# Optimization experiments

Measured on AMD Instinct MI355X. Metric: run time of the kernel, lower is better.

The kernel has to match this reference:

```python
import jax, jax.numpy as jnp
import numpy as np

HORIZON = 1024
N_EMBD = 256
N_LAYER = 4
ACTION_DIM = 10
DIM = 64
ACT_NUM = 10
N_POS = 4 * (1 + HORIZON)
FEAT = 3 + DIM * ACT_NUM + ACTION_DIM  # 653
EPS = 1e-5
BATCH = 8


def _layernorm(x, g, b):
    m = jnp.mean(x, axis=-1, keepdims=True)
    v = jnp.mean((x - m) ** 2, axis=-1, keepdims=True)
    return (x - m) * jax.lax.rsqrt(v + EPS) * g + b


def setup_inputs() -> dict:
    key = jax.random.key(0)
    ks = jax.random.split(key, 16)
    f = jnp.float32
    L, E = N_LAYER, N_EMBD
    return {
        'query_states': jax.random.normal(ks[0], (BATCH, 64), f),
        'action_set': jax.random.normal(ks[1], (BATCH, ACT_NUM, DIM), f),
        'context_actions': jax.random.normal(ks[2], (BATCH, HORIZON, ACTION_DIM), f),
        'context_rewards': jax.random.normal(ks[3], (BATCH, HORIZON, 1), f),
        'W_embed': jax.random.normal(ks[4], (FEAT, E), f) * 0.02,
        'b_embed': jnp.zeros((E,), f),
        'wpe': jax.random.normal(ks[5], (N_POS, E), f) * 0.02,
        'Wq': jax.random.normal(ks[6], (L, E, E), f) * 0.02,
        'Wk': jax.random.normal(ks[7], (L, E, E), f) * 0.02,
        'Wv': jax.random.normal(ks[8], (L, E, E), f) * 0.02,
        'ln1_g': jnp.ones((L, E), f),
        'ln1_b': jnp.zeros((L, E), f),
        'W1': jax.random.normal(ks[9], (L, E, E), f) * 0.02,
        'b1': jnp.zeros((L, E), f),
        'W2': jax.random.normal(ks[10], (L, E, E), f) * 0.02,
        'b2': jnp.zeros((L, E), f),
        'ln2_g': jnp.ones((L, E), f),
        'ln2_b': jnp.zeros((L, E), f),
        'W_pred': jax.random.normal(ks[11], (E, ACTION_DIM), f) * 0.02,
        'b_pred': jnp.zeros((ACTION_DIM,), f),
    }


def reference(query_states, action_set, context_actions, context_rewards,
              W_embed, b_embed, wpe, Wq, Wk, Wv,
              ln1_g, ln1_b, W1, b1, W2, b2, ln2_g, ln2_b,
              W_pred, b_pred):
    B = action_set.shape[0]
    T = context_actions.shape[1]
    A = context_actions.shape[2]
    N = 2 * T
    # --- build the interleaved sequence (test=False path) ---
    aset0 = action_set.reshape(B, 1, -1)                         # [B,1,dim*act_num]
    aset = jnp.concatenate([aset0, jnp.zeros_like(aset0)], axis=1)  # [B,2,F0]
    aset = jnp.tile(aset, (1, T, 1))                              # [B,2T,F0]
    action_seq = jnp.zeros((B, N, A + 1), dtype=context_actions.dtype)
    action_seq = action_seq.at[:, 1::2, :].set(
        jnp.concatenate([context_actions, context_rewards], axis=2))
    one_seq = jnp.ones((B, N, 1), dtype=context_actions.dtype)
    pos_seq = jnp.broadcast_to(
        jnp.arange(1, N + 1, dtype=context_actions.dtype).reshape(1, N, 1), (B, N, 1))
    seq = jnp.concatenate([aset, action_seq, one_seq, pos_seq], axis=2)  # [B,N,FEAT]
    # --- embed + positional embedding ---
    H = seq @ W_embed + b_embed          # [B,N,E]
    H = H + wpe[:N]                       # position_ids = arange(N)
    # --- causal mask with per-row 1/(i+1) normalization ---
    i = jnp.arange(N)[:, None]
    j = jnp.arange(N)[None, :]
    mask = jnp.where(j <= i, 1.0 / (i + 1).astype(H.dtype), 0.0)  # [N,N]
    # --- decoder layers: relu(QK^T)*mask attention + MLP, layernorms ---
    for l in range(N_LAYER):
        q = H @ Wq[l]
        k = H @ Wk[l]
        v = H @ Wv[l]
        attn = jax.nn.relu(jnp.einsum('bid,bjd->bij', q, k)) * mask  # [B,N,N]
        H = H + jnp.einsum('bij,bjd->bid', attn, v)
        H = _layernorm(H, ln1_g[l], ln1_b[l])
        H = H + jax.nn.relu(H @ W1[l] + b1[l]) @ W2[l] + b2[l]
        H = _layernorm(H, ln2_g[l], ln2_b[l])
    preds = H @ W_pred + b_pred           # [B,N,action_dim]
    return preds[:, 0::2, :]              # [B,T,action_dim]
```

## Files before the change

kernel.cpp:

```cpp
#include <hip/hip_runtime.h>


#define BB 8
#define TT 1024
#define NN 2048
#define EE 256
#define LL 4

typedef __attribute__((ext_vector_type(8))) short short8;
typedef __attribute__((ext_vector_type(4))) float f32x4;

__device__ inline ushort f2b(float f) {
    union { float f; unsigned u; } x; x.f = f;
    unsigned u = x.u;
    return (ushort)((u + 0x7fffu + ((u >> 16) & 1u)) >> 16);
}
__device__ inline unsigned cvtpk(float lo, float hi) {
    unsigned r;
    asm volatile("v_cvt_pk_bf16_f32 %0, %1, %2" : "=v"(r) : "v"(lo), "v"(hi));
    return r;
}
__device__ inline size_t pk256(int row, int k) {
    return ((size_t)((row >> 4) * 8 + (k >> 5))) * 512
         + (size_t)((((k >> 3) & 3) * 16 + (row & 15)) * 8 + (k & 7));
}
__device__ inline size_t vpk_idx(int bb, int nn, int e) {
    return ((size_t)(bb*64 + (nn >> 5)) * 16 + (e >> 4)) * 512
         + (size_t)((((nn >> 3) & 3) * 16 + (e & 15)) * 8 + (nn & 7));
}

__global__ __launch_bounds__(256) void wprep_k(
    const float* __restrict__ Wq, const float* __restrict__ Wk,
    const float* __restrict__ Wv, const float* __restrict__ W1,
    const float* __restrict__ W2,
    ushort* __restrict__ WQKt, ushort* __restrict__ WVt,
    ushort* __restrict__ W1t, ushort* __restrict__ W2t)
{
    int id = blockIdx.x;
    int m = id >> 4, t = id & 15;
    int l = m / 5, which = m % 5;
    const float* src; ushort* dst;
    size_t o = (size_t)l * 65536;
    switch (which) {
        case 0: src = Wq + o; dst = WQKt + (size_t)l*131072;          break;
        case 1: src = Wk + o; dst = WQKt + (size_t)l*131072 + 65536;  break;
        case 2: src = Wv + o; dst = WVt + o; break;
        case 3: src = W1 + o; dst = W1t + o; break;
        default: src = W2 + o; dst = W2t + o; break;
    }
    int tk = (t >> 2) * 64;
    int tn = (t & 3) * 64;
    __shared__ ushort T[64][68];
    int tid = threadIdx.x;
    int r = tid >> 4, c4 = (tid & 15) * 4;
    #pragma unroll
    for (int it = 0; it < 4; ++it) {
        int k = r + it*16;
        float4 v = *(const float4*)&src[(size_t)(tk + k)*256 + tn + c4];
        T[k][c4+0] = f2b(v.x); T[k][c4+1] = f2b(v.y);
        T[k][c4+2] = f2b(v.z); T[k][c4+3] = f2b(v.w);
    }
    __syncthreads();
    #pragma unroll
    for (int it = 0; it < 4; ++it) {
        int n = tn + r + it*16;
        int k0 = tk + c4;
        ushort4 ov;
        ov.x = T[c4+0][n-tn]; ov.y = T[c4+1][n-tn];
        ov.z = T[c4+2][n-tn]; ov.w = T[c4+3][n-tn];
        *(ushort4*)&dst[pk256(n, k0)] = ov;
    }
}

__global__ __launch_bounds__(256) void base_even_k(
    const float* __restrict__ aset, const float* __restrict__ We,
    const float* __restrict__ be, float* __restrict__ BE)
{
    int b = blockIdx.x; int e = threadIdx.x;
    __shared__ float as[640];
    for (int i = e; i < 640; i += 256) as[i] = aset[b*640 + i];
    __syncthreads();
    float s = We[651*EE + e] + be[e];
    for (int f = 0; f < 640; ++f) s = fmaf(as[f], We[f*EE + e], s);
    BE[b*EE + e] = s;
}

__global__ __launch_bounds__(256) void embed_k(
    const float* __restrict__ BE, const float* __restrict__ ca,
    const float* __restrict__ cr, const float* __restrict__ We,
    const float* __restrict__ be, const float* __restrict__ wpe,
    float* __restrict__ H, ushort* __restrict__ Hbf)
{
    int e = threadIdx.x;
    #pragma unroll
    for (int k = 0; k < 8; ++k) {
        int rb = blockIdx.x * 8 + k;
        int b = rb >> 11, n = rb & (NN-1);
        float h;
        if ((n & 1) == 0) {
            h = BE[b*EE + e];
        } else {
            int t = n >> 1;
            h = We[651*EE + e] + be[e];
            const float* cap = ca + (size_t)(b*TT + t)*10;
            #pragma unroll
            for (int i = 0; i < 10; ++i) h = fmaf(cap[i], We[(640+i)*EE + e], h);
            h = fmaf(cr[b*TT + t], We[650*EE + e], h);
        }
        h = fmaf((float)(n + 1), We[652*EE + e], h);
        h += wpe[(size_t)n*EE + e];
        H[(size_t)rb*EE + e] = h;
        Hbf[pk256(rb, e)] = f2b(h);
    }
}

__global__ __launch_bounds__(256, 2) void qkv_k(
    const ushort* __restrict__ A, const ushort* __restrict__ WQK,
    const ushort* __restrict__ WV,
    ushort* __restrict__ Qo, ushort* __restrict__ Ko, ushort* __restrict__ Vo)
{
    int tid = threadIdx.x;
    int w = tid >> 6, l = tid & 63;
    int lr = l & 15, lg = l >> 4;
    int wr = w >> 1, wc = w & 1;
    int rt0 = blockIdx.x * 8 + wr*4;
    int ct0 = blockIdx.y * 8 + wc*4;
    const ushort* Ap = A + (size_t)rt0*4096 + l*8;
    const ushort* Bp = (blockIdx.y < 4 ? WQK + (size_t)ct0*4096
                                       : WV + (size_t)(ct0-32)*4096) + l*8;
    f32x4 acc[4][4];
    #pragma unroll
    for (int i = 0; i < 4; ++i)
        #pragma unroll
        for (int j = 0; j < 4; ++j) acc[i][j] = (f32x4){0.f,0.f,0.f,0.f};
    #pragma unroll
    for (int kc = 0; kc < 8; ++kc) {
        short8 af[4], bf[4];
        #pragma unroll
        for (int rg = 0; rg < 4; ++rg) af[rg] = *(const short8*)(Ap + (size_t)rg*4096 + kc*512);
        #pragma unroll
        for (int cg = 0; cg < 4; ++cg) bf[cg] = *(const short8*)(Bp + (size_t)cg*4096 + kc*512);
        #pragma unroll
        for (int rg = 0; rg < 4; ++rg)
            #pragma unroll
            for (int cg = 0; cg < 4; ++cg)
                acc[rg][cg] = __builtin_amdgcn_mfma_f32_16x16x32_bf16(af[rg], bf[cg], acc[rg][cg], 0,0,0);
    }
    #pragma unroll
    for (int rg = 0; rg < 4; ++rg)
        #pragma unroll
        for (int cg = 0; cg < 4; ++cg)
            #pragma unroll
            for (int r = 0; r < 4; ++r) {
                int row = rt0*16 + rg*16 + lg*4 + r;
                int col = ct0*16 + cg*16 + lr;
                ushort xv = f2b(acc[rg][cg][r]);
                if (col < 256)      Qo[pk256(row, col)] = xv;
                else if (col < 512) Ko[pk256(row, col - 256)] = xv;
                else {
                    int e = col - 512, bb = row >> 11, nn = row & (NN-1);
                    Vo[vpk_idx(bb, nn, e)] = xv;
                }
            }
}

__global__ __launch_bounds__(256, 2) void mlp1_k(
    const ushort* __restrict__ A, const ushort* __restrict__ Bw,
    const float* __restrict__ bias, ushort* __restrict__ Cv)
{
    int tid = threadIdx.x;
    int w = tid >> 6, l = tid & 63;
    int lr = l & 15, lg = l >> 4;
    int wr = w >> 1, wc = w & 1;
    int rt0 = blockIdx.x * 8 + wr*4;
    int ct0 = blockIdx.y * 8 + wc*4;
    const ushort* Ap = A  + (size_t)rt0*4096 + l*8;
    const ushort* Bp = Bw + (size_t)ct0*4096 + l*8;
    f32x4 acc[4][4];
    #pragma unroll
    for (int i = 0; i < 4; ++i)
        #pragma unroll
        for (int j = 0; j < 4; ++j) acc[i][j] = (f32x4){0.f,0.f,0.f,0.f};
    #pragma unroll
    for (int kc = 0; kc < 8; ++kc) {
        short8 af[4], bf[4];
        #pragma unroll
        for (int rg = 0; rg < 4; ++rg) af[rg] = *(const short8*)(Ap + (size_t)rg*4096 + kc*512);
        #pragma unroll
        for (int cg = 0; cg < 4; ++cg) bf[cg] = *(const short8*)(Bp + (size_t)cg*4096 + kc*512);
        #pragma unroll
        for (int rg = 0; rg < 4; ++rg)
            #pragma unroll
            for (int cg = 0; cg < 4; ++cg)
                acc[rg][cg] = __builtin_amdgcn_mfma_f32_16x16x32_bf16(af[rg], bf[cg], acc[rg][cg], 0,0,0);
    }
    #pragma unroll
    for (int rg = 0; rg < 4; ++rg)
        #pragma unroll
        for (int cg = 0; cg < 4; ++cg)
            #pragma unroll
            for (int r = 0; r < 4; ++r) {
                int row = rt0*16 + rg*16 + lg*4 + r;
                int col = ct0*16 + cg*16 + lr;
                float x = fmaxf(acc[rg][cg][r] + bias[col], 0.f);
                Cv[pk256(row, col)] = f2b(x);
            }
}

__global__ __launch_bounds__(256, 2) void mlp2ln_k(
    const ushort* __restrict__ A, const ushort* __restrict__ Bw,
    const float* __restrict__ bias, const float* __restrict__ Res,
    const float* __restrict__ g, const float* __restrict__ bt,
    float* __restrict__ Hout, ushort* __restrict__ Hpk)
{
    int tid = threadIdx.x;
    int w = tid >> 6, l = tid & 63;
    int lr = l & 15, lg = l >> 4;
    int rt0 = blockIdx.x * 2;
    int ct0 = w * 4;
    const ushort* Ap = A  + (size_t)rt0*4096 + l*8;
    const ushort* Bp = Bw + (size_t)ct0*4096 + l*8;
    f32x4 acc[2][4];
    #pragma unroll
    for (int i = 0; i < 2; ++i)
        #pragma unroll
        for (int j = 0; j < 4; ++j) acc[i][j] = (f32x4){0.f,0.f,0.f,0.f};
    #pragma unroll
    for (int kc = 0; kc < 8; ++kc) {
        short8 a0 = *(const short8*)(Ap + kc*512);
        short8 a1 = *(const short8*)(Ap + 4096 + kc*512);
        short8 bf[4];
        #pragma unroll
        for (int cg = 0; cg < 4; ++cg) bf[cg] = *(const short8*)(Bp + (size_t)cg*4096 + kc*512);
        #pragma unroll
        for (int cg = 0; cg < 4; ++cg) {
            acc[0][cg] = __builtin_amdgcn_mfma_f32_16x16x32_bf16(a0, bf[cg], acc[0][cg], 0,0,0);
            acc[1][cg] = __builtin_amdgcn_mfma_f32_16x16x32_bf16(a1, bf[cg], acc[1][cg], 0,0,0);
        }
    }
    __shared__ float red[32][4][2];
    float sm[2][4] = {}, sq[2][4] = {};
    #pragma unroll
    for (int rg = 0; rg < 2; ++rg)
        #pragma unroll
        for (int cg = 0; cg < 4; ++cg)
            #pragma unroll
            for (int r = 0; r < 4; ++r) {
                int grow = blockIdx.x*32 + rg*16 + lg*4 + r;
                int col = w*64 + cg*16 + lr;
                float v = acc[rg][cg][r] + bias[col] + Res[(size_t)grow*EE + col];
                acc[rg][cg][r] = v;
                sm[rg][r] += v; sq[rg][r] += v*v;
            }
    #pragma unroll
    for (int off = 1; off < 16; off <<= 1)
        #pragma unroll
        for (int rg = 0; rg < 2; ++rg)
            #pragma unroll
            for (int r = 0; r < 4; ++r) {
                sm[rg][r] += __shfl_xor(sm[rg][r], off);
                sq[rg][r] += __shfl_xor(sq[rg][r], off);
            }
    if (lr == 0) {
        #pragma unroll
        for (int rg = 0; rg < 2; ++rg)
            #pragma unroll
            for (int r = 0; r < 4; ++r) {
                int rl = rg*16 + lg*4 + r;
                red[rl][w][0] = sm[rg][r];
                red[rl][w][1] = sq[rg][r];
            }
    }
    __syncthreads();
    #pragma unroll
    for (int rg = 0; rg < 2; ++rg)
        #pragma unroll
        for (int r = 0; r < 4; ++r) {
            int rl = rg*16 + lg*4 + r;
            float S  = red[rl][0][0] + red[rl][1][0] + red[rl][2][0] + red[rl][3][0];
            float S2 = red[rl][0][1] + red[rl][1][1] + red[rl][2][1] + red[rl][3][1];
            float mean = S * (1.0f/256.0f);
            float var  = S2 * (1.0f/256.0f) - mean*mean;
            float inv  = 1.0f / sqrtf(var + 1e-5f);
            int grow = blockIdx.x*32 + rl;
            #pragma unroll
            for (int cg = 0; cg < 4; ++cg) {
                int col = w*64 + cg*16 + lr;
                float y = (acc[rg][cg][r] - mean) * inv * g[col] + bt[col];
                Hout[(size_t)grow*EE + col] = y;
                Hpk[pk256(grow, col)] = f2b(y);
            }
        }
}

__global__ __launch_bounds__(512, 2) void attn_k(
    const ushort* __restrict__ Qp, const ushort* __restrict__ Kp,
    const ushort* __restrict__ Vp, const float* __restrict__ H,
    const float* __restrict__ g, const float* __restrict__ bt,
    float* __restrict__ Xout, ushort* __restrict__ Lpk)
{
    int blk = blockIdx.x;
    int pk = blk >> 3, b = blk & 7;
    int tid = threadIdx.x;
    int w = tid >> 6, l = tid & 63;
    int lr = l & 15, lg = l >> 4;
    int sel  = (w & 1) ^ ((w >> 2) & 1);
    int part = w >> 1;
    int s  = sel ? (127 - pk) : pk;
    int i0 = s * 16;
    int NT = (s >> 1) + 1;
    int j0 = (part * NT) >> 2;
    int j1 = ((part + 1) * NT) >> 2;

    __shared__ float comb[2][5440];

    const ushort* Qt    = Qp + (size_t)(b*128 + s) * 4096 + l*8;
    const ushort* Kbase = Kp + (size_t)(b*128) * 4096 + l*8;
    const ushort* Vbase = Vp + (size_t)(b*64) * 16 * 512 + l*8;

    short8 qb[8];
    #pragma unroll
    for (int kc = 0; kc < 8; ++kc) qb[kc] = *(const short8*)(Qt + kc*512);

    f32x4 oacc[16];
    #pragma unroll
    for (int et = 0; et < 16; ++et) oacc[et] = (f32x4){0.f,0.f,0.f,0.f};

    int ig = i0 + lr;
    for (int jt = j0; jt < j1; ++jt) {
        const ushort* Kt = Kbase + (size_t)(jt*2) * 4096;
        short8 ka0[8], ka1[8];
        #pragma unroll
        for (int kc = 0; kc < 8; ++kc) {
            ka0[kc] = *(const short8*)(Kt + kc*512);
            ka1[kc] = *(const short8*)(Kt + 4096 + kc*512);
        }
        const ushort* Vt = Vbase + (size_t)(jt*16) * 512;
        short8 vf[16];
        #pragma unroll
        for (int et = 0; et < 16; ++et)
            vf[et] = *(const short8*)(Vt + et*512);
        f32x4 c0a = {0.f,0.f,0.f,0.f}, c0b = {0.f,0.f,0.f,0.f};
        f32x4 c1a = {0.f,0.f,0.f,0.f}, c1b = {0.f,0.f,0.f,0.f};
        #pragma unroll
        for (int kc = 0; kc < 8; kc += 2) {
            c0a = __builtin_amdgcn_mfma_f32_16x16x32_bf16(ka0[kc],   qb[kc],   c0a, 0,0,0);
            c0b = __builtin_amdgcn_mfma_f32_16x16x32_bf16(ka0[kc+1], qb[kc+1], c0b, 0,0,0);
            c1a = __builtin_amdgcn_mfma_f32_16x16x32_bf16(ka1[kc],   qb[kc],   c1a, 0,0,0);
            c1b = __builtin_amdgcn_mfma_f32_16x16x32_bf16(ka1[kc+1], qb[kc+1], c1b, 0,0,0);
        }
        f32x4 c0 = c0a + c0b, c1 = c1a + c1b;
        #pragma unroll
        for (int r = 0; r < 4; ++r) {
            int jg = jt*32 + lg*4 + r;
            c0[r] = (jg <= ig) ? fmaxf(c0[r], 0.f) : 0.f;
            c1[r] = (jg + 16 <= ig) ? fmaxf(c1[r], 0.f) : 0.f;
        }
        unsigned u0 = cvtpk(c0[0], c0[1]), u1 = cvtpk(c0[2], c0[3]);
        unsigned u2 = cvtpk(c1[0], c1[1]), u3 = cvtpk(c1[2], c1[3]);
        int srcA = 32*(lg & 1) + lr;
        int srcB = srcA + 16;
        unsigned a0A = __shfl((int)u0, srcA), a1A = __shfl((int)u1, srcA);
        unsigned a0B = __shfl((int)u0, srcB), a1B = __shfl((int)u1, srcB);
        unsigned b0A = __shfl((int)u2, srcA), b1A = __shfl((int)u3, srcA);
        unsigned b0B = __shfl((int)u2, srcB), b1B = __shfl((int)u3, srcB);
        bool lo = (lg < 2);
        union { unsigned u[4]; short8 v; } sv;
        sv.u[0] = lo ? a0A : b0A;
        sv.u[1] = lo ? a1A : b1A;
        sv.u[2] = lo ? a0B : b0B;
        sv.u[3] = lo ? a1B : b1B;
        short8 sa = sv.v;
        __builtin_amdgcn_s_setprio(1);
        #pragma unroll
        for (int et = 0; et < 16; ++et)
            oacc[et] = __builtin_amdgcn_mfma_f32_16x16x32_bf16(sa, vf[et], oacc[et], 0,0,0);
        __builtin_amdgcn_s_setprio(0);
    }

    float* cb = &comb[sel][0];
    #pragma unroll
    for (int rnd = 1; rnd <= 3; ++rnd) {
        if (part == rnd) {
            #pragma unroll
            for (int et = 0; et < 16; ++et)
                #pragma unroll
                for (int r = 0; r < 4; ++r) {
                    int idx = et*340 + l*5 + r;
                    float v = oacc[et][r];
                    if (rnd == 1) cb[idx] = v; else cb[idx] += v;
                }
        }
        __syncthreads();
    }
    if (part == 0) {
        float sm[4] = {0.f,0.f,0.f,0.f}, sq[4] = {0.f,0.f,0.f,0.f};
        #pragma unroll
        for (int et = 0; et < 16; ++et)
            #pragma unroll
            for (int r = 0; r < 4; ++r) {
                int irow = i0 + lg*4 + r;
                size_t base = ((size_t)(b*NN + irow))*EE + et*16 + lr;
                float x = H[base] + (oacc[et][r] + cb[et*340 + l*5 + r])
                                    * (1.0f / (float)(irow + 1));
                oacc[et][r] = x;
                sm[r] += x; sq[r] += x*x;
            }
        #pragma unroll
        for (int off = 1; off < 16; off <<= 1)
            #pragma unroll
            for (int r = 0; r < 4; ++r) {
                sm[r] += __shfl_xor(sm[r], off);
                sq[r] += __shfl_xor(sq[r], off);
            }
        float mean[4], inv[4];
        #pragma unroll
        for (int r = 0; r < 4; ++r) {
            mean[r] = sm[r] * (1.0f/256.0f);
            float var = sq[r] * (1.0f/256.0f) - mean[r]*mean[r];
            inv[r] = 1.0f / sqrtf(var + 1e-5f);
        }
        #pragma unroll
        for (int et = 0; et < 16; ++et) {
            int col = et*16 + lr;
            float gv = g[col], bv = bt[col];
            #pragma unroll
            for (int r = 0; r < 4; ++r) {
                int irow = i0 + lg*4 + r;
                size_t base = ((size_t)(b*NN + irow))*EE + col;
                float y = (oacc[et][r] - mean[r]) * inv[r] * gv + bv;
                Xout[base] = y;
                Lpk[pk256(b*NN + irow, col)] = f2b(y);
            }
        }
    }
}

__global__ __launch_bounds__(256) void pred_k(
    const float* __restrict__ H, const float* __restrict__ Wp,
    const float* __restrict__ bp, float* __restrict__ out)
{
    int bt = blockIdx.x;
    int b = bt >> 10, t = bt & 1023;
    size_t row = (size_t)b*NN + 2*t;
    __shared__ float hs[256];
    __shared__ float pr[16][16];
    int tid = threadIdx.x;
    hs[tid] = H[row*EE + tid];
    __syncthreads();
    int c = tid & 15, seg = tid >> 4;
    float p = 0.f;
    if (c < 10) {
        #pragma unroll
        for (int e2 = 0; e2 < 16; ++e2)
            p = fmaf(hs[seg*16 + e2], Wp[(seg*16 + e2)*10 + c], p);
    }
    pr[seg][c] = p;
    __syncthreads();
    if (tid < 10) {
        float sacc = bp[tid];
        #pragma unroll
        for (int k2 = 0; k2 < 16; ++k2) sacc += pr[k2][tid];
        out[(size_t)bt*10 + tid] = sacc;
    }
}

extern "C" void kernel_launch(void* const* d_in, const int* in_sizes, int n_in,
                              void* d_out, int out_size, void* d_ws, size_t ws_size,
                              hipStream_t stream)
{
    const float* action_set = (const float*)d_in[1];
    const float* ctx_act    = (const float*)d_in[2];
    const float* ctx_rew    = (const float*)d_in[3];
    const float* W_embed    = (const float*)d_in[4];
    const float* b_embed    = (const float*)d_in[5];
    const float* wpe        = (const float*)d_in[6];
    const float* Wq         = (const float*)d_in[7];
    const float* Wk         = (const float*)d_in[8];
    const float* Wv         = (const float*)d_in[9];
    const float* ln1g       = (const float*)d_in[10];
    const float* ln1b       = (const float*)d_in[11];
    const float* W1         = (const float*)d_in[12];
    const float* b1         = (const float*)d_in[13];
    const float* W2         = (const float*)d_in[14];
    const float* b2         = (const float*)d_in[15];
    const float* ln2g       = (const float*)d_in[16];
    const float* ln2b       = (const float*)d_in[17];
    const float* Wp         = (const float*)d_in[18];
    const float* bp         = (const float*)d_in[19];
    float* out = (float*)d_out;

    float* ws = (float*)d_ws;
    const size_t SZ = (size_t)BB*NN*EE;
    size_t o = 0;
    float*  Hb   = ws;               o += SZ;
    float*  Xb   = ws + o;           o += SZ;
    ushort* Hbf  = (ushort*)(ws+o);  o += SZ/2;
    ushort* Qp   = (ushort*)(ws+o);  o += SZ/2;
    ushort* Kpk  = (ushort*)(ws+o);  o += SZ/2;
    ushort* Vpk  = (ushort*)(ws+o);  o += SZ/2;
    ushort* WQKt = (ushort*)(ws+o);  o += 262144;
    ushort* WVt  = (ushort*)(ws+o);  o += 131072;
    ushort* W1t  = (ushort*)(ws+o);  o += 131072;
    ushort* W2t  = (ushort*)(ws+o);  o += 131072;
    float*  BE   = ws + o;

    wprep_k<<<320, 256, 0, stream>>>(Wq, Wk, Wv, W1, W2, WQKt, WVt, W1t, W2t);
    base_even_k<<<BB, 256, 0, stream>>>(action_set, W_embed, b_embed, BE);
    embed_k<<<BB*NN/8, 256, 0, stream>>>(BE, ctx_act, ctx_rew, W_embed, b_embed, wpe, Hb, Hbf);

    for (int l = 0; l < LL; ++l) {
        qkv_k<<<dim3(128, 6), 256, 0, stream>>>(
            Hbf, WQKt + (size_t)l*131072, WVt + (size_t)l*65536, Qp, Kpk, Vpk);
        attn_k<<<512, 512, 0, stream>>>(
            Qp, Kpk, Vpk, Hb, ln1g + l*EE, ln1b + l*EE, Xb, Hbf);
        mlp1_k<<<dim3(128, 2), 256, 0, stream>>>(
            Hbf, W1t + (size_t)l*65536, b1 + l*EE, Qp);
        mlp2ln_k<<<512, 256, 0, stream>>>(
            Qp, W2t + (size_t)l*65536, b2 + l*EE, Xb,
            ln2g + l*EE, ln2b + l*EE, Hb, Hbf);
    }
    pred_k<<<BB*TT, 256, 0, stream>>>(Hb, Wp, bp, out);
}
```

Before: 446.3 us.

## Split causal attention into two halves and move residual+LayerNorm into separate kernel

The attention kernel changes from 512-thread blocks with four waves splitting the key range and combining through shared memory to 256-thread blocks. Each block now covers a 64-row query group, and its key range is cut into two halves written to two fp32 partial buffers. A new comb_ln1_k kernel adds the partials, applies the 1/(i+1) scale and residual, and does LayerNorm with vectorized loads. This removes the in-block shared-memory reduction and its barriers and rebalances work across blocks. In exchange it adds an extra kernel launch per layer and two full fp32 activation round trips through global memory, and puts a __syncthreads inside the key loop.

```diff
diff --git a/kernel.cpp b/kernel.cpp
--- a/kernel.cpp
+++ b/kernel.cpp
@@ -293,30 +293,27 @@
         }
 }
 
-__global__ __launch_bounds__(512, 2) void attn_k(
+__global__ __launch_bounds__(256, 2) void attn_k(
     const ushort* __restrict__ Qp, const ushort* __restrict__ Kp,
-    const ushort* __restrict__ Vp, const float* __restrict__ H,
-    const float* __restrict__ g, const float* __restrict__ bt,
-    float* __restrict__ Xout, ushort* __restrict__ Lpk)
-{
-    int blk = blockIdx.x;
-    int pk = blk >> 3, b = blk & 7;
+    const ushort* __restrict__ Vp, float* __restrict__ Oa,
+    float* __restrict__ Ob)
+{
+    int bi = blockIdx.x;
+    int h = bi >> 8;
+    int j = bi & 255;
+    int b = j >> 5;
+    int p = h ? (31 - (j & 31)) : (j & 31);
     int tid = threadIdx.x;
     int w = tid >> 6, l = tid & 63;
     int lr = l & 15, lg = l >> 4;
-    int sel  = (w & 1) ^ ((w >> 2) & 1);
-    int part = w >> 1;
-    int s  = sel ? (127 - pk) : pk;
-    int i0 = s * 16;
-    int NT = (s >> 1) + 1;
-    int j0 = (part * NT) >> 2;
-    int j1 = ((part + 1) * NT) >> 2;
-
-    __shared__ float comb[2][5440];
-
-    const ushort* Qt    = Qp + (size_t)(b*128 + s) * 4096 + l*8;
-    const ushort* Kbase = Kp + (size_t)(b*128) * 4096 + l*8;
-    const ushort* Vbase = Vp + (size_t)(b*64) * 16 * 512 + l*8;
+    int i0 = p*64 + w*16;
+    int j0 = h ? (p + 1) : 0;
+    int j1 = h ? (2*p + 2) : (p + 1);
+    float* Op = h ? Ob : Oa;
+
+    const ushort* Qt    = Qp + (size_t)(b*128 + p*4 + w)*4096 + l*8;
+    const ushort* Kbase = Kp + (size_t)(b*128)*4096 + l*8;
+    const ushort* Vbase = Vp + (size_t)(b*64)*16*512 + l*8;
 
     short8 qb[8];
     #pragma unroll
@@ -376,64 +373,53 @@
         for (int et = 0; et < 16; ++et)
             oacc[et] = __builtin_amdgcn_mfma_f32_16x16x32_bf16(sa, vf[et], oacc[et], 0,0,0);
         __builtin_amdgcn_s_setprio(0);
-    }
-
-    float* cb = &comb[sel][0];
-    #pragma unroll
-    for (int rnd = 1; rnd <= 3; ++rnd) {
-        if (part == rnd) {
-            #pragma unroll
-            for (int et = 0; et < 16; ++et)
-                #pragma unroll
-                for (int r = 0; r < 4; ++r) {
-                    int idx = et*340 + l*5 + r;
-                    float v = oacc[et][r];
-                    if (rnd == 1) cb[idx] = v; else cb[idx] += v;
-                }
-        }
         __syncthreads();
     }
-    if (part == 0) {
-        float sm[4] = {0.f,0.f,0.f,0.f}, sq[4] = {0.f,0.f,0.f,0.f};
-        #pragma unroll
-        for (int et = 0; et < 16; ++et)
-            #pragma unroll
-            for (int r = 0; r < 4; ++r) {
-                int irow = i0 + lg*4 + r;
-                size_t base = ((size_t)(b*NN + irow))*EE + et*16 + lr;
-                float x = H[base] + (oacc[et][r] + cb[et*340 + l*5 + r])
-                                    * (1.0f / (float)(irow + 1));
-                oacc[et][r] = x;
-                sm[r] += x; sq[r] += x*x;
-            }
-        #pragma unroll
-        for (int off = 1; off < 16; off <<= 1)
-            #pragma unroll
-            for (int r = 0; r < 4; ++r) {
-                sm[r] += __shfl_xor(sm[r], off);
-                sq[r] += __shfl_xor(sq[r], off);
-            }
-        float mean[4], inv[4];
+    #pragma unroll
+    for (int et = 0; et < 16; ++et)
         #pragma unroll
         for (int r = 0; r < 4; ++r) {
-            mean[r] = sm[r] * (1.0f/256.0f);
-            float var = sq[r] * (1.0f/256.0f) - mean[r]*mean[r];
-            inv[r] = 1.0f / sqrtf(var + 1e-5f);
-        }
-        #pragma unroll
-        for (int et = 0; et < 16; ++et) {
-            int col = et*16 + lr;
-            float gv = g[col], bv = bt[col];
-            #pragma unroll
-            for (int r = 0; r < 4; ++r) {
-                int irow = i0 + lg*4 + r;
-                size_t base = ((size_t)(b*NN + irow))*EE + col;
-                float y = (oacc[et][r] - mean[r]) * inv[r] * gv + bv;
-                Xout[base] = y;
-                Lpk[pk256(b*NN + irow, col)] = f2b(y);
-            }
-        }
-    }
+            int irow = i0 + lg*4 + r;
+            Op[((size_t)(b*NN + irow))*EE + et*16 + lr] = oacc[et][r];
+        }
+}
+
+__global__ __launch_bounds__(256) void comb_ln1_k(
+    const float* Oa, const float* __restrict__ Ob,
+    const float* __restrict__ H, const float* __restrict__ g,
+    const float* __restrict__ bt, float* Xout, ushort* __restrict__ Lpk)
+{
+    int w = threadIdx.x >> 6, l = threadIdx.x & 63;
+    size_t row = (size_t)blockIdx.x*4 + w;
+    float sc = 1.0f / (float)((row & (NN-1)) + 1);
+    float4 oa = *(const float4*)&Oa[row*EE + l*4];
+    float4 ob = *(const float4*)&Ob[row*EE + l*4];
+    float4 hh = *(const float4*)&H[row*EE + l*4];
+    float4 x;
+    x.x = hh.x + (oa.x + ob.x)*sc;
+    x.y = hh.y + (oa.y + ob.y)*sc;
+    x.z = hh.z + (oa.z + ob.z)*sc;
+    x.w = hh.w + (oa.w + ob.w)*sc;
+    float s  = x.x + x.y + x.z + x.w;
+    float s2 = x.x*x.x + x.y*x.y + x.z*x.z + x.w*x.w;
+    #pragma unroll
+    for (int off = 1; off < 64; off <<= 1) {
+        s  += __shfl_xor(s,  off);
+        s2 += __shfl_xor(s2, off);
+    }
+    float mean = s * (1.0f/256.0f);
+    float var  = s2 * (1.0f/256.0f) - mean*mean;
+    float inv  = 1.0f / sqrtf(var + 1e-5f);
+    float4 gv = *(const float4*)&g[l*4];
+    float4 bv = *(const float4*)&bt[l*4];
+    float4 y;
+    y.x = (x.x - mean)*inv*gv.x + bv.x;
+    y.y = (x.y - mean)*inv*gv.y + bv.y;
+    y.z = (x.z - mean)*inv*gv.z + bv.z;
+    y.w = (x.w - mean)*inv*gv.w + bv.w;
+    *(float4*)&Xout[row*EE + l*4] = y;
+    ushort4 yb; yb.x = f2b(y.x); yb.y = f2b(y.y); yb.z = f2b(y.z); yb.w = f2b(y.w);
+    *(ushort4*)&Lpk[pk256((int)row, l*4)] = yb;
 }
 
 __global__ __launch_bounds__(256) void pred_k(
@@ -495,6 +481,7 @@
     size_t o = 0;
     float*  Hb   = ws;               o += SZ;
     float*  Xb   = ws + o;           o += SZ;
+    float*  Obuf = ws + o;           o += SZ;
     ushort* Hbf  = (ushort*)(ws+o);  o += SZ/2;
     ushort* Qp   = (ushort*)(ws+o);  o += SZ/2;
     ushort* Kpk  = (ushort*)(ws+o);  o += SZ/2;
@@ -512,8 +499,9 @@
     for (int l = 0; l < LL; ++l) {
         qkv_k<<<dim3(128, 6), 256, 0, stream>>>(
             Hbf, WQKt + (size_t)l*131072, WVt + (size_t)l*65536, Qp, Kpk, Vpk);
-        attn_k<<<512, 512, 0, stream>>>(
-            Qp, Kpk, Vpk, Hb, ln1g + l*EE, ln1b + l*EE, Xb, Hbf);
+        attn_k<<<512, 256, 0, stream>>>(Qp, Kpk, Vpk, Xb, Obuf);
+        comb_ln1_k<<<BB*NN/4, 256, 0, stream>>>(
+            Xb, Obuf, Hb, ln1g + l*EE, ln1b + l*EE, Xb, Hbf);
         mlp1_k<<<dim3(128, 2), 256, 0, stream>>>(
             Hbf, W1t + (size_t)l*65536, b1 + l*EE, Qp);
         mlp2ln_k<<<512, 256, 0, stream>>>(
```

Measured after the change: 490.6 us. 1.1x slower.

## Restructure attention so four row-waves share key/value tiles in lockstep

Applied to the files above, without the earlier changes.

The attention kernel now gives each block 64 consecutive query rows: four waves of 16 rows, with two halves splitting the causal key range. Previously each block paired a short and a long 16-row strip across four key-range partitions. A barrier inside the key loop keeps the four waves on the same K/V tile, so loads can be reused through cache, and the cross-partition reduction becomes a single LDS exchange. The grid is halved, launch bounds allow one block per CU, and the old short/long pairing is gone, so per-block work now grows with row position and the load may be unbalanced.

```diff
diff --git a/kernel.cpp b/kernel.cpp
--- a/kernel.cpp
+++ b/kernel.cpp
@@ -293,30 +293,26 @@
         }
 }
 
-__global__ __launch_bounds__(512, 2) void attn_k(
+__global__ __launch_bounds__(512, 1) void attn_k(
     const ushort* __restrict__ Qp, const ushort* __restrict__ Kp,
     const ushort* __restrict__ Vp, const float* __restrict__ H,
     const float* __restrict__ g, const float* __restrict__ bt,
     float* __restrict__ Xout, ushort* __restrict__ Lpk)
 {
     int blk = blockIdx.x;
-    int pk = blk >> 3, b = blk & 7;
+    int p = blk >> 3, b = blk & 7;
     int tid = threadIdx.x;
     int w = tid >> 6, l = tid & 63;
     int lr = l & 15, lg = l >> 4;
-    int sel  = (w & 1) ^ ((w >> 2) & 1);
-    int part = w >> 1;
-    int s  = sel ? (127 - pk) : pk;
-    int i0 = s * 16;
-    int NT = (s >> 1) + 1;
-    int j0 = (part * NT) >> 2;
-    int j1 = ((part + 1) * NT) >> 2;
-
-    __shared__ float comb[2][5440];
-
-    const ushort* Qt    = Qp + (size_t)(b*128 + s) * 4096 + l*8;
-    const ushort* Kbase = Kp + (size_t)(b*128) * 4096 + l*8;
-    const ushort* Vbase = Vp + (size_t)(b*64) * 16 * 512 + l*8;
+    int h = w >> 2, w4 = w & 3;
+    int i0 = p*64 + w4*16;
+    int jbase = h * (p + 1);
+
+    __shared__ float comb[4][16][256];
+
+    const ushort* Qt    = Qp + (size_t)(b*128 + p*4 + w4)*4096 + l*8;
+    const ushort* Kbase = Kp + (size_t)(b*128)*4096 + l*8;
+    const ushort* Vbase = Vp + (size_t)(b*64)*16*512 + l*8;
 
     short8 qb[8];
     #pragma unroll
@@ -327,15 +323,16 @@
     for (int et = 0; et < 16; ++et) oacc[et] = (f32x4){0.f,0.f,0.f,0.f};
 
     int ig = i0 + lr;
-    for (int jt = j0; jt < j1; ++jt) {
-        const ushort* Kt = Kbase + (size_t)(jt*2) * 4096;
+    for (int jt = 0; jt <= p; ++jt) {
+        int jte = jbase + jt;
+        const ushort* Kt = Kbase + (size_t)(jte*2) * 4096;
         short8 ka0[8], ka1[8];
         #pragma unroll
         for (int kc = 0; kc < 8; ++kc) {
             ka0[kc] = *(const short8*)(Kt + kc*512);
             ka1[kc] = *(const short8*)(Kt + 4096 + kc*512);
         }
-        const ushort* Vt = Vbase + (size_t)(jt*16) * 512;
+        const ushort* Vt = Vbase + (size_t)(jte*16) * 512;
         short8 vf[16];
         #pragma unroll
         for (int et = 0; et < 16; ++et)
@@ -352,7 +349,7 @@
         f32x4 c0 = c0a + c0b, c1 = c1a + c1b;
         #pragma unroll
         for (int r = 0; r < 4; ++r) {
-            int jg = jt*32 + lg*4 + r;
+            int jg = jte*32 + lg*4 + r;
             c0[r] = (jg <= ig) ? fmaxf(c0[r], 0.f) : 0.f;
             c1[r] = (jg + 16 <= ig) ? fmaxf(c1[r], 0.f) : 0.f;
         }
@@ -376,24 +373,18 @@
         for (int et = 0; et < 16; ++et)
             oacc[et] = __builtin_amdgcn_mfma_f32_16x16x32_bf16(sa, vf[et], oacc[et], 0,0,0);
         __builtin_amdgcn_s_setprio(0);
-    }
-
-    float* cb = &comb[sel][0];
-    #pragma unroll
-    for (int rnd = 1; rnd <= 3; ++rnd) {
-        if (part == rnd) {
-            #pragma unroll
-            for (int et = 0; et < 16; ++et)
-                #pragma unroll
-                for (int r = 0; r < 4; ++r) {
-                    int idx = et*340 + l*5 + r;
-                    float v = oacc[et][r];
-                    if (rnd == 1) cb[idx] = v; else cb[idx] += v;
-                }
-        }
         __syncthreads();
     }
-    if (part == 0) {
+
+    if (h == 1) {
+        #pragma unroll
+        for (int et = 0; et < 16; ++et)
+            #pragma unroll
+            for (int r = 0; r < 4; ++r)
+                comb[w4][lg*4 + r][et*16 + lr] = oacc[et][r];
+    }
+    __syncthreads();
+    if (h == 0) {
         float sm[4] = {0.f,0.f,0.f,0.f}, sq[4] = {0.f,0.f,0.f,0.f};
         #pragma unroll
         for (int et = 0; et < 16; ++et)
@@ -401,8 +392,8 @@
             for (int r = 0; r < 4; ++r) {
                 int irow = i0 + lg*4 + r;
                 size_t base = ((size_t)(b*NN + irow))*EE + et*16 + lr;
-                float x = H[base] + (oacc[et][r] + cb[et*340 + l*5 + r])
-                                    * (1.0f / (float)(irow + 1));
+                float o = oacc[et][r] + comb[w4][lg*4 + r][et*16 + lr];
+                float x = H[base] + o * (1.0f / (float)(irow + 1));
                 oacc[et][r] = x;
                 sm[r] += x; sq[r] += x*x;
             }
@@ -512,7 +503,7 @@
     for (int l = 0; l < LL; ++l) {
         qkv_k<<<dim3(128, 6), 256, 0, stream>>>(
             Hbf, WQKt + (size_t)l*131072, WVt + (size_t)l*65536, Qp, Kpk, Vpk);
-        attn_k<<<512, 512, 0, stream>>>(
+        attn_k<<<256, 512, 0, stream>>>(
             Qp, Kpk, Vpk, Hb, ln1g + l*EE, ln1b + l*EE, Xb, Hbf);
         mlp1_k<<<dim3(128, 2), 256, 0, stream>>>(
             Hbf, W1t + (size_t)l*65536, b1 + l*EE, Qp);
```

Measured after the change: 546.9 us. +22.6%, slower.

## Process 32 query rows per wave in attention to reuse K/V fragments

Applied to the files above, without the earlier changes.

The attention kernel now gives each wave two 16-row query tiles (32 rows) instead of one, so every K and V fragment loaded from global memory feeds twice as many MFMAs. The grid is halved to 256 blocks, and the shared-memory combine buffer is resized and re-laid-out row-major for 32 rows. K and V are now loaded inside the MFMA loops rather than preloaded into registers. The intent is to halve K/V traffic per unit of work, at the cost of twice the accumulator registers (possible spills or lower occupancy), fewer blocks for the GPU's CUs, and less latency hiding.

```diff
diff --git a/kernel.cpp b/kernel.cpp
--- a/kernel.cpp
+++ b/kernel.cpp
@@ -306,75 +306,90 @@
     int lr = l & 15, lg = l >> 4;
     int sel  = (w & 1) ^ ((w >> 2) & 1);
     int part = w >> 1;
-    int s  = sel ? (127 - pk) : pk;
-    int i0 = s * 16;
-    int NT = (s >> 1) + 1;
+    int z  = sel ? (63 - pk) : pk;
+    int i0 = z * 32;
+    int NT = z + 1;
     int j0 = (part * NT) >> 2;
     int j1 = ((part + 1) * NT) >> 2;
 
-    __shared__ float comb[2][5440];
-
-    const ushort* Qt    = Qp + (size_t)(b*128 + s) * 4096 + l*8;
+    __shared__ float comb[2][32 * 260];
+
+    const ushort* Qt    = Qp + (size_t)(b*128 + z*2) * 4096 + l*8;
     const ushort* Kbase = Kp + (size_t)(b*128) * 4096 + l*8;
     const ushort* Vbase = Vp + (size_t)(b*64) * 16 * 512 + l*8;
 
-    short8 qb[8];
-    #pragma unroll
-    for (int kc = 0; kc < 8; ++kc) qb[kc] = *(const short8*)(Qt + kc*512);
-
-    f32x4 oacc[16];
-    #pragma unroll
-    for (int et = 0; et < 16; ++et) oacc[et] = (f32x4){0.f,0.f,0.f,0.f};
-
-    int ig = i0 + lr;
+    short8 qa[8], qb[8];
+    #pragma unroll
+    for (int kc = 0; kc < 8; ++kc) {
+        qa[kc] = *(const short8*)(Qt + kc*512);
+        qb[kc] = *(const short8*)(Qt + 4096 + kc*512);
+    }
+
+    f32x4 oa[16], ob[16];
+    #pragma unroll
+    for (int et = 0; et < 16; ++et) {
+        oa[et] = (f32x4){0.f,0.f,0.f,0.f};
+        ob[et] = (f32x4){0.f,0.f,0.f,0.f};
+    }
+
+    int ig0 = i0 + lr;
+    int ig1 = i0 + 16 + lr;
     for (int jt = j0; jt < j1; ++jt) {
         const ushort* Kt = Kbase + (size_t)(jt*2) * 4096;
-        short8 ka0[8], ka1[8];
+        const ushort* Vt = Vbase + (size_t)(jt*16) * 512;
+        f32x4 c0 = {0.f,0.f,0.f,0.f}, c1 = {0.f,0.f,0.f,0.f};
+        f32x4 d0 = {0.f,0.f,0.f,0.f}, d1 = {0.f,0.f,0.f,0.f};
         #pragma unroll
         for (int kc = 0; kc < 8; ++kc) {
-            ka0[kc] = *(const short8*)(Kt + kc*512);
-            ka1[kc] = *(const short8*)(Kt + 4096 + kc*512);
-        }
-        const ushort* Vt = Vbase + (size_t)(jt*16) * 512;
-        short8 vf[16];
-        #pragma unroll
-        for (int et = 0; et < 16; ++et)
-            vf[et] = *(const short8*)(Vt + et*512);
-        f32x4 c0a = {0.f,0.f,0.f,0.f}, c0b = {0.f,0.f,0.f,0.f};
-        f32x4 c1a = {0.f,0.f,0.f,0.f}, c1b = {0.f,0.f,0.f,0.f};
-        #pragma unroll
-        for (int kc = 0; kc < 8; kc += 2) {
-            c0a = __builtin_amdgcn_mfma_f32_16x16x32_bf16(ka0[kc],   qb[kc],   c0a, 0,0,0);
-            c0b = __builtin_amdgcn_mfma_f32_16x16x32_bf16(ka0[kc+1], qb[kc+1], c0b, 0,0,0);
-            c1a = __builtin_amdgcn_mfma_f32_16x16x32_bf16(ka1[kc],   qb[kc],   c1a, 0,0,0);
-            c1b = __builtin_amdgcn_mfma_f32_16x16x32_bf16(ka1[kc+1], qb[kc+1], c1b, 0,0,0);
-        }
-        f32x4 c0 = c0a + c0b, c1 = c1a + c1b;
+            short8 k0 = *(const short8*)(Kt + kc*512);
+            short8 k1 = *(const short8*)(Kt + 4096 + kc*512);
+            c0 = __builtin_amdgcn_mfma_f32_16x16x32_bf16(k0, qa[kc], c0, 0,0,0);
+            c1 = __builtin_amdgcn_mfma_f32_16x16x32_bf16(k1, qa[kc], c1, 0,0,0);
+            d0 = __builtin_amdgcn_mfma_f32_16x16x32_bf16(k0, qb[kc], d0, 0,0,0);
+            d1 = __builtin_amdgcn_mfma_f32_16x16x32_bf16(k1, qb[kc], d1, 0,0,0);
+        }
         #pragma unroll
         for (int r = 0; r < 4; ++r) {
             int jg = jt*32 + lg*4 + r;
-            c0[r] = (jg <= ig) ? fmaxf(c0[r], 0.f) : 0.f;
-            c1[r] = (jg + 16 <= ig) ? fmaxf(c1[r], 0.f) : 0.f;
-        }
+            c0[r] = (jg <= ig0)      ? fmaxf(c0[r], 0.f) : 0.f;
+            c1[r] = (jg + 16 <= ig0) ? fmaxf(c1[r], 0.f) : 0.f;
+            d0[r] = (jg <= ig1)      ? fmaxf(d0[r], 0.f) : 0.f;
+            d1[r] = (jg + 16 <= ig1) ? fmaxf(d1[r], 0.f) : 0.f;
+        }
+        int srcA = 32*(lg & 1) + lr;
+        int srcB = srcA + 16;
+        bool lo = (lg < 2);
         unsigned u0 = cvtpk(c0[0], c0[1]), u1 = cvtpk(c0[2], c0[3]);
         unsigned u2 = cvtpk(c1[0], c1[1]), u3 = cvtpk(c1[2], c1[3]);
-        int srcA = 32*(lg & 1) + lr;
-        int srcB = srcA + 16;
         unsigned a0A = __shfl((int)u0, srcA), a1A = __shfl((int)u1, srcA);
         unsigned a0B = __shfl((int)u0, srcB), a1B = __shfl((int)u1, srcB);
         unsigned b0A = __shfl((int)u2, srcA), b1A = __shfl((int)u3, srcA);
         unsigned b0B = __shfl((int)u2, srcB), b1B = __shfl((int)u3, srcB);
-        bool lo = (lg < 2);
-        union { unsigned u[4]; short8 v; } sv;
-        sv.u[0] = lo ? a0A : b0A;
-        sv.u[1] = lo ? a1A : b1A;
-        sv.u[2] = lo ? a0B : b0B;
-        sv.u[3] = lo ? a1B : b1B;
-        short8 sa = sv.v;
+        union { unsigned u[4]; short8 v; } sv0;
+        sv0.u[0] = lo ? a0A : b0A;
+        sv0.u[1] = lo ? a1A : b1A;
+        sv0.u[2] = lo ? a0B : b0B;
+        sv0.u[3] = lo ? a1B : b1B;
+        short8 sa = sv0.v;
+        unsigned v0 = cvtpk(d0[0], d0[1]), v1 = cvtpk(d0[2], d0[3]);
+        unsigned v2 = cvtpk(d1[0], d1[1]), v3 = cvtpk(d1[2], d1[3]);
+        unsigned c0A = __shfl((int)v0, srcA), c1A = __shfl((int)v1, srcA);
+        unsigned c0B = __shfl((int)v0, srcB), c1B = __shfl((int)v1, srcB);
+        unsigned d0A = __shfl((int)v2, srcA), d1A = __shfl((int)v3, srcA);
+        unsigned d0B = __shfl((int)v2, srcB), d1B = __shfl((int)v3, srcB);
+        union { unsigned u[4]; short8 v; } sv1;
+        sv1.u[0] = lo ? c0A : d0A;
+        sv1.u[1] = lo ? c1A : d1A;
+        sv1.u[2] = lo ? c0B : d0B;
+        sv1.u[3] = lo ? c1B : d1B;
+        short8 sb = sv1.v;
         __builtin_amdgcn_s_setprio(1);
         #pragma unroll
-        for (int et = 0; et < 16; ++et)
-            oacc[et] = __builtin_amdgcn_mfma_f32_16x16x32_bf16(sa, vf[et], oacc[et], 0,0,0);
+        for (int et = 0; et < 16; ++et) {
+            short8 vf = *(const short8*)(Vt + et*512);
+            oa[et] = __builtin_amdgcn_mfma_f32_16x16x32_bf16(sa, vf, oa[et], 0,0,0);
+            ob[et] = __builtin_amdgcn_mfma_f32_16x16x32_bf16(sb, vf, ob[et], 0,0,0);
+        }
         __builtin_amdgcn_s_setprio(0);
     }
 
@@ -386,53 +401,61 @@
             for (int et = 0; et < 16; ++et)
                 #pragma unroll
                 for (int r = 0; r < 4; ++r) {
-                    int idx = et*340 + l*5 + r;
-                    float v = oacc[et][r];
-                    if (rnd == 1) cb[idx] = v; else cb[idx] += v;
+                    int ia = (lg*4 + r)*260 + et*16 + lr;
+                    int ib = (16 + lg*4 + r)*260 + et*16 + lr;
+                    if (rnd == 1) { cb[ia] = oa[et][r];  cb[ib] = ob[et][r]; }
+                    else          { cb[ia] += oa[et][r]; cb[ib] += ob[et][r]; }
                 }
         }
         __syncthreads();
     }
     if (part == 0) {
-        float sm[4] = {0.f,0.f,0.f,0.f}, sq[4] = {0.f,0.f,0.f,0.f};
-        #pragma unroll
-        for (int et = 0; et < 16; ++et)
-            #pragma unroll
-            for (int r = 0; r < 4; ++r) {
-                int irow = i0 + lg*4 + r;
-                size_t base = ((size_t)(b*NN + irow))*EE + et*16 + lr;
-                float x = H[base] + (oacc[et][r] + cb[et*340 + l*5 + r])
-                                    * (1.0f / (float)(irow + 1));
-                oacc[et][r] = x;
-                sm[r] += x; sq[r] += x*x;
-            }
-        #pragma unroll
-        for (int off = 1; off < 16; off <<= 1)
-            #pragma unroll
-            for (int r = 0; r < 4; ++r) {
-                sm[r] += __shfl_xor(sm[r], off);
-                sq[r] += __shfl_xor(sq[r], off);
-            }
-        float mean[4], inv[4];
-        #pragma unroll
-        for (int r = 0; r < 4; ++r) {
-            mean[r] = sm[r] * (1.0f/256.0f);
-            float var = sq[r] * (1.0f/256.0f) - mean[r]*mean[r];
-            inv[r] = 1.0f / sqrtf(var + 1e-5f);
-        }
-        #pragma unroll
-        for (int et = 0; et < 16; ++et) {
-            int col = et*16 + lr;
-            float gv = g[col], bv = bt[col];
-            #pragma unroll
-            for (int r = 0; r < 4; ++r) {
-                int irow = i0 + lg*4 + r;
-                size_t base = ((size_t)(b*NN + irow))*EE + col;
-                float y = (oacc[et][r] - mean[r]) * inv[r] * gv + bv;
-                Xout[base] = y;
-                Lpk[pk256(b*NN + irow, col)] = f2b(y);
-            }
-        }
+#define EPILOG(SET, OACC)                                                      \
+        {                                                                      \
+            float sm[4] = {0.f,0.f,0.f,0.f}, sq[4] = {0.f,0.f,0.f,0.f};        \
+            _Pragma("unroll")                                                  \
+            for (int et = 0; et < 16; ++et)                                    \
+                _Pragma("unroll")                                              \
+                for (int r = 0; r < 4; ++r) {                                  \
+                    int irow = i0 + SET*16 + lg*4 + r;                         \
+                    size_t base = ((size_t)(b*NN + irow))*EE + et*16 + lr;     \
+                    float o = OACC[et][r]                                      \
+                            + cb[(SET*16 + lg*4 + r)*260 + et*16 + lr];        \
+                    float x = H[base] + o * (1.0f / (float)(irow + 1));        \
+                    OACC[et][r] = x;                                           \
+                    sm[r] += x; sq[r] += x*x;                                  \
+                }                                                              \
+            _Pragma("unroll")                                                  \
+            for (int off = 1; off < 16; off <<= 1)                             \
+                _Pragma("unroll")                                              \
+                for (int r = 0; r < 4; ++r) {                                  \
+                    sm[r] += __shfl_xor(sm[r], off);                           \
+                    sq[r] += __shfl_xor(sq[r], off);                           \
+                }                                                              \
+            float mean[4], inv[4];                                             \
+            _Pragma("unroll")                                                  \
+            for (int r = 0; r < 4; ++r) {                                      \
+                mean[r] = sm[r] * (1.0f/256.0f);                               \
+                float var = sq[r] * (1.0f/256.0f) - mean[r]*mean[r];           \
+                inv[r] = 1.0f / sqrtf(var + 1e-5f);                            \
+            }                                                                  \
+            _Pragma("unroll")                                                  \
+            for (int et = 0; et < 16; ++et) {                                  \
+                int col = et*16 + lr;                                          \
+                float gv = g[col], bv = bt[col];                               \
+                _Pragma("unroll")                                              \
+                for (int r = 0; r < 4; ++r) {                                  \
+                    int irow = i0 + SET*16 + lg*4 + r;                         \
+                    size_t base = ((size_t)(b*NN + irow))*EE + col;            \
+                    float y = (OACC[et][r] - mean[r]) * inv[r] * gv + bv;      \
+                    Xout[base] = y;                                            \
+                    Lpk[pk256(b*NN + irow, col)] = f2b(y);                     \
+                }                                                              \
+            }                                                                  \
+        }
+        EPILOG(0, oa)
+        EPILOG(1, ob)
+#undef EPILOG
     }
 }
 
@@ -512,7 +535,7 @@
     for (int l = 0; l < LL; ++l) {
         qkv_k<<<dim3(128, 6), 256, 0, stream>>>(
             Hbf, WQKt + (size_t)l*131072, WVt + (size_t)l*65536, Qp, Kpk, Vpk);
-        attn_k<<<512, 512, 0, stream>>>(
+        attn_k<<<256, 512, 0, stream>>>(
             Qp, Kpk, Vpk, Hb, ln1g + l*EE, ln1b + l*EE, Xb, Hbf);
         mlp1_k<<<dim3(128, 2), 256, 0, stream>>>(
             Hbf, W1t + (size_t)l*65536, b1 + l*EE, Qp);
```

New measurement: 636.4 us. 42.6% more time.
